# Optimization experiments

Hardware: AMD Instinct MI355X
Metric: run time of the kernel (lower is better)

Reference implementation:

```python
import jax, jax.numpy as jnp
import numpy as np

B, N, D, K = 16, 1024, 512, 8
NUM_ITERS = 3
EPS = 1e-08
LN_EPS = 1e-05


def layer_norm(x, g, b):
    m = jnp.mean(x, axis=-1, keepdims=True)
    v = jnp.var(x, axis=-1, keepdims=True)
    return (x - m) * jax.lax.rsqrt(v + LN_EPS) * g + b


def setup_inputs() -> dict:
    key = jax.random.key(0)
    ks = jax.random.split(key, 8)
    s = 1.0 / np.sqrt(D)
    return {
        "embeddings": jax.random.normal(ks[0], (B, N, D), jnp.float32),
        "noise_init": jax.random.normal(ks[1], (B, K, D), jnp.float32),
        "noise_final": jax.random.normal(ks[2], (B, K, D), jnp.float32),
        "slots_mu": jax.random.normal(ks[3], (1, K, D), jnp.float32) * s,
        "slots_logsigma": jax.random.normal(ks[4], (1, K, D), jnp.float32) * s,
        "mixing_coeffs": jnp.ones((1, K), jnp.float32) / K,
        "Wk": jax.random.normal(ks[5], (D, D), jnp.float32) * s,
        "bk": jnp.zeros((D,), jnp.float32),
        "Wq": jax.random.normal(ks[6], (D, D), jnp.float32) * s,
        "bq": jnp.zeros((D,), jnp.float32),
        "Wv": jax.random.normal(ks[7], (D, D), jnp.float32) * s,
        "bv": jnp.zeros((D,), jnp.float32),
        "ln_g": jnp.ones((D,), jnp.float32),
        "ln_b": jnp.zeros((D,), jnp.float32),
    }


def reference(embeddings, noise_init, noise_final, slots_mu, slots_logsigma,
              mixing_coeffs, Wk, bk, Wq, bq, Wv, bv, ln_g, ln_b):
    b, n, d = embeddings.shape
    mixing = jnp.broadcast_to(mixing_coeffs, (b, K))           # [B,K]
    mu = jnp.broadcast_to(slots_mu, (b, K, d))                 # [B,K,D]
    sigma = jnp.exp(jnp.broadcast_to(slots_logsigma, (b, K, d)))
    slots = mu + sigma * noise_init                            # sampled slots

    x = layer_norm(embeddings, ln_g, ln_b)
    keys = x @ Wk + bk                                         # [B,N,D]
    values = x @ Wv + bv                                       # [B,N,D]
    # slots are never updated inside the loop, so queries are loop-invariant
    queries = slots @ Wq + bq                                  # [B,K,D]

    log2pi = jnp.float32(np.log(2.0 * np.pi))
    attn = None
    for _ in range(NUM_ITERS):
        diff = keys[:, :, None, :] - queries[:, None, :, :]    # [B,N,K,D]
        gll = -0.5 * jnp.sum(diff * diff / (sigma[:, None] ** 2 + EPS), axis=-1)  # [B,N,K]
        gll = (-0.5 * d * log2pi
               - 0.5 * jnp.sum(jnp.log(jnp.abs(sigma) + EPS), axis=-1)[:, None, :]
               + gll)
        attn = mixing[:, None, :] * gll                        # [B,N,K]
        attn = attn / jnp.sum(attn, axis=-1, keepdims=True)
        attn = attn / (jnp.sum(attn, axis=1, keepdims=True) + EPS)
        mu = jnp.einsum('bnk,bnd->bkd', attn, values)          # [B,K,D]
        diff2 = values[:, :, None, :] - mu[:, None, :, :]      # [B,N,K,D]
        sigma = jnp.einsum('bnk,bnkd->bkd', attn, diff2 * diff2)
        mixing = jnp.sum(attn, axis=1) / n

    sigma = jnp.maximum(jnp.abs(sigma), EPS)
    slots = mu + sigma * noise_final
    return slots, jnp.transpose(attn, (0, 2, 1))
```

## Files before the change

kernel.cpp:

```cpp
#include <hip/hip_runtime.h>
#include <math.h>

#define BB 16
#define NN 1024
#define DD 512
#define KK 8
#define EPS_ 1e-8f
#define LN_EPS_ 1e-5f
#define GLL_C0 (-470.4965290007924f)

typedef __attribute__((ext_vector_type(8))) short short8;
typedef __attribute__((ext_vector_type(4))) short short4v;
typedef __attribute__((ext_vector_type(4))) float f32x4;

static __device__ inline short f2bf(float f) {
    unsigned u = __builtin_bit_cast(unsigned, f);
    u = (u + 0x7fff + ((u >> 16) & 1)) >> 16;
    return (short)u;
}
static __device__ inline float bf2f(short s) {
    unsigned u = ((unsigned)(unsigned short)s) << 16;
    return __builtin_bit_cast(float, u);
}

static __device__ inline void gload16(const void* g, void* l) {
    __builtin_amdgcn_global_load_lds(
        (const __attribute__((address_space(1))) void*)g,
        (__attribute__((address_space(3))) void*)l, 16, 0, 0);
}

__global__ __launch_bounds__(256) void pre_kernel(
    const float* __restrict__ emb, const float* __restrict__ lng,
    const float* __restrict__ lnb, short* __restrict__ Abf,
    const float* __restrict__ Wk, const float* __restrict__ Wv,
    const float* __restrict__ Wq, short* __restrict__ WtKV, short* __restrict__ WqT,
    const float* __restrict__ noise_init, const float* __restrict__ slots_mu,
    const float* __restrict__ slots_logsigma, short* __restrict__ slots_bf)
{
    int bid = blockIdx.x;
    int tid = threadIdx.x;
    if (bid < 4096) {
        int row  = bid * 4 + (tid >> 6);
        int lane = tid & 63;
        const float* e = emb + (size_t)row * DD + lane * 8;
        float4 v0 = *(const float4*)e;
        float4 v1 = *(const float4*)(e + 4);
        float v[8] = {v0.x, v0.y, v0.z, v0.w, v1.x, v1.y, v1.z, v1.w};
        float s = 0.0f;
#pragma unroll
        for (int j = 0; j < 8; j++) s += v[j];
#pragma unroll
        for (int off = 32; off; off >>= 1) s += __shfl_xor(s, off);
        float m = s * (1.0f / DD);
        float vs = 0.0f;
#pragma unroll
        for (int j = 0; j < 8; j++) { float d = v[j] - m; vs = fmaf(d, d, vs); }
#pragma unroll
        for (int off = 32; off; off >>= 1) vs += __shfl_xor(vs, off);
        float rstd = rsqrtf(vs * (1.0f / DD) + LN_EPS_);

        float4 g0 = *(const float4*)&lng[lane * 8];
        float4 g1 = *(const float4*)&lng[lane * 8 + 4];
        float4 b0 = *(const float4*)&lnb[lane * 8];
        float4 b1 = *(const float4*)&lnb[lane * 8 + 4];
        float g[8] = {g0.x, g0.y, g0.z, g0.w, g1.x, g1.y, g1.z, g1.w};
        float bb[8] = {b0.x, b0.y, b0.z, b0.w, b1.x, b1.y, b1.z, b1.w};
        short8 o;
#pragma unroll
        for (int j = 0; j < 8; j++) o[j] = f2bf(fmaf((v[j] - m) * rstd, g[j], bb[j]));
        *(short8*)&Abf[(size_t)row * DD + lane * 8] = o;
    } else if (bid < 4864) {
        int idx = bid - 4096;
        int z = idx >> 8, rem = idx & 255;
        const float* W = (z == 0) ? Wk : (z == 1) ? Wv : Wq;
        short* T; int nbase;
        if (z < 2) { T = WtKV; nbase = z * 512; } else { T = WqT; nbase = 0; }
        int k0 = (rem & 15) * 32, n0 = (rem >> 4) * 32;
        int tx = tid & 31, ty = tid >> 5;
        __shared__ float t[32][33];
#pragma unroll
        for (int p = 0; p < 4; p++)
            t[ty + p * 8][tx] = W[(size_t)(k0 + ty + p * 8) * DD + n0 + tx];
        __syncthreads();
#pragma unroll
        for (int p = 0; p < 4; p++)
            T[(size_t)(nbase + n0 + ty + p * 8) * DD + k0 + tx] = f2bf(t[tx][ty + p * 8]);
    } else {
        int idx = bid - 4864;
        int b = idx >> 3, k = idx & 7;
#pragma unroll
        for (int q = 0; q < 2; q++) {
            int d = tid + q * 256;
            float sg = expf(slots_logsigma[k * DD + d]);
            float sl = fmaf(sg, noise_init[((size_t)(b * KK + k)) * DD + d],
                            slots_mu[k * DD + d]);
            slots_bf[((size_t)(b * KK + k)) * DD + d] = f2bf(sl);
        }
    }
}

__global__ __launch_bounds__(256) void gemm_mfma_kernel(
    const short* __restrict__ Abf, const short* __restrict__ slotbf,
    const short* __restrict__ WtKV, const short* __restrict__ WqT,
    const float* __restrict__ bk, const float* __restrict__ bv,
    const float* __restrict__ bq,
    short* __restrict__ E, short* __restrict__ Vbf, float* __restrict__ Cq)
{
    int x = blockIdx.x, by = blockIdx.y;
    const short* A; const short* Bt;
    int qmode = 0, row0 = 0;
    if (by == 128) {
        if (x >= 4) return;
        A = slotbf; Bt = WqT; qmode = 1;
    } else {
        A = Abf + (size_t)by * 128 * DD;
        Bt = WtKV;
        row0 = by * 128;
    }

    __shared__ short As[128 * 64];
    __shared__ short Bs[128 * 64];

    int tid = threadIdx.x;
    int w = tid >> 6, l = tid & 63;
    int col0 = x * 128;

    int sr = l >> 3;
    int sg_off = ((l & 7) ^ sr) * 8;

    int mq = (w & 1) * 64, nq = (w >> 1) * 64;
    int fr = l & 15;

    f32x4 acc[4][4] = {};

    for (int k0 = 0; k0 < DD; k0 += 64) {
        __syncthreads();
#pragma unroll
        for (int j = 0; j < 4; j++) {
            int rb = w * 32 + j * 8;
            int r  = rb + sr;
            gload16(A  + (size_t)r * DD + k0 + sg_off, &As[rb * 64 + l * 8]);
            gload16(Bt + (size_t)(col0 + r) * DD + k0 + sg_off, &Bs[rb * 64 + l * 8]);
        }
        __syncthreads();

#pragma unroll
        for (int kk = 0; kk < 2; kk++) {
            int g = kk * 4 + (l >> 4);
            short8 af[4], bfv[4];
#pragma unroll
            for (int mi = 0; mi < 4; mi++) {
                int row = mq + mi * 16 + fr;
                af[mi] = *(const short8*)&As[row * 64 + (g ^ (fr & 7)) * 8];
            }
#pragma unroll
            for (int ni = 0; ni < 4; ni++) {
                int row = nq + ni * 16 + fr;
                bfv[ni] = *(const short8*)&Bs[row * 64 + (g ^ (fr & 7)) * 8];
            }
#pragma unroll
            for (int mi = 0; mi < 4; mi++)
#pragma unroll
                for (int ni = 0; ni < 4; ni++)
                    acc[mi][ni] = __builtin_amdgcn_mfma_f32_16x16x32_bf16(
                        af[mi], bfv[ni], acc[mi][ni], 0, 0, 0);
        }
    }

    int orow = (l >> 4) * 4, ocol = l & 15;
#pragma unroll
    for (int ni = 0; ni < 4; ni++) {
        int col = col0 + nq + ni * 16 + ocol;
        float bv_ = qmode ? bq[col] : (col < 512 ? bk[col] : bv[col - 512]);
#pragma unroll
        for (int mi = 0; mi < 4; mi++) {
#pragma unroll
            for (int r = 0; r < 4; r++) {
                int row = row0 + mq + mi * 16 + orow + r;
                float val = acc[mi][ni][r] + bv_;
                if (qmode) {
                    Cq[(size_t)row * DD + col] = val;
                } else if (col < 512) {
                    E[(size_t)row * 1024 + col]       = f2bf(val * val);
                    E[(size_t)row * 1024 + 512 + col] = f2bf(val);
                } else {
                    Vbf[(size_t)row * DD + (col - 512)] = f2bf(val);
                }
            }
        }
    }
}

__global__ __launch_bounds__(256) void fprep0_kernel(
    const float* __restrict__ slots_logsigma, const float* __restrict__ queries,
    const float* __restrict__ mixing_coeffs, short* __restrict__ F_bt,
    float* __restrict__ off, float* __restrict__ mix16, float* __restrict__ colsum)
{
    int b = blockIdx.x, k = blockIdx.y;
    int tid = threadIdx.x;
    short* Fr = F_bt + (size_t)(b * 16 + k) * 1024;
    if (k >= KK) {
        short4v zv = {0, 0, 0, 0};
        *(short4v*)&Fr[tid * 4] = zv;
        if (tid == 0) { off[b * 16 + k] = 0.0f; mix16[b * 16 + k] = 0.0f; }
        return;
    }
    float c = 0.0f, ld = 0.0f;
#pragma unroll
    for (int q = 0; q < 2; q++) {
        int d = tid * 2 + q;
        float sg = expf(slots_logsigma[k * DD + d]);
        float iv = 1.0f / (sg * sg + EPS_);
        float qv = queries[((size_t)(b * KK + k)) * DD + d];
        Fr[d]       = f2bf(-0.5f * iv);
        Fr[512 + d] = f2bf(qv * iv);
        c  = fmaf(qv * qv, iv, c);
        ld += logf(fabsf(sg) + EPS_);
    }
    __shared__ float rc[256], rl[256];
    rc[tid] = c; rl[tid] = ld;
    __syncthreads();
    for (int s = 128; s > 0; s >>= 1) {
        if (tid < s) { rc[tid] += rc[tid + s]; rl[tid] += rl[tid + s]; }
        __syncthreads();
    }
    if (tid == 0) {
        off[b * 16 + k]    = GLL_C0 - 0.5f * rl[0] - 0.5f * rc[0];
        mix16[b * 16 + k]  = mixing_coeffs[k];
        colsum[b * KK + k] = 0.0f;
    }
}

__global__ __launch_bounds__(256) void gll_mfma_kernel(
    const short* __restrict__ E, const short* __restrict__ F_bt,
    const float* __restrict__ off, const float* __restrict__ mix16,
    float* __restrict__ attn, float* __restrict__ colsum)
{
    int b = blockIdx.y;
    int tid = threadIdx.x;
    int w = tid >> 6, l = tid & 63;
    int m0 = blockIdx.x * 16;

    const short* Ea = E + ((size_t)(b * NN + m0 + (l & 15))) * 1024 + (l >> 4) * 8;
    const short* Fa = F_bt + (size_t)(b * 16 + (l & 15)) * 1024 + (l >> 4) * 8;

    f32x4 acc = {};
    int kbase = w * 256;
#pragma unroll
    for (int j = 0; j < 8; j++) {
        int k0 = kbase + j * 32;
        short8 af = *(const short8*)&Ea[k0];
        short8 bf = *(const short8*)&Fa[k0];
        acc = __builtin_amdgcn_mfma_f32_16x16x32_bf16(af, bf, acc, 0, 0, 0);
    }

    __shared__ f32x4 red[3][64];
    if (w) red[w - 1][l] = acc;
    __syncthreads();
    if (w) return;
#pragma unroll
    for (int i = 0; i < 3; i++) acc += red[i][l];

    int col = l & 15;
    int rbase = m0 + (l >> 4) * 4;
    float offv = off[b * 16 + col];
    float mixv = mix16[b * 16 + col];

    float a[4], den[4];
#pragma unroll
    for (int r = 0; r < 4; r++) {
        a[r] = mixv * (acc[r] + offv);
        den[r] = a[r];
    }
#pragma unroll
    for (int mask = 1; mask <= 8; mask <<= 1)
#pragma unroll
        for (int r = 0; r < 4; r++) den[r] += __shfl_xor(den[r], mask);

    float csl = 0.0f;
    if (col < KK) {
#pragma unroll
        for (int r = 0; r < 4; r++) {
            float v = a[r] / den[r];
            attn[((size_t)(b * NN + rbase + r)) * KK + col] = v;
            csl += v;
        }
    }
    csl += __shfl_xor(csl, 16);
    csl += __shfl_xor(csl, 32);
    if (l < KK) atomicAdd(&colsum[b * KK + l], csl);
}

__global__ __launch_bounds__(256) void musigma_kernel(
    const short* __restrict__ Vbf, const float* __restrict__ attn,
    float* __restrict__ s1p, float* __restrict__ s2p)
{
    int b = blockIdx.x, ns = blockIdx.y;
    int tid = threadIdx.x;
    int d0 = tid * 2;
    __shared__ float asml[64 * KK];
    const float* ab = attn + ((size_t)(b * NN + ns * 64)) * KK;
    if (tid < 128) ((float4*)asml)[tid] = ((const float4*)ab)[tid];
    __syncthreads();

    float s1[2][KK] = {}, s2[2][KK] = {};
    const short* vb = Vbf + ((size_t)(b * NN + ns * 64)) * DD + d0;
#pragma unroll 4
    for (int nn = 0; nn < 64; nn++) {
        short2 vs = *(const short2*)&vb[(size_t)nn * DD];
        float v0 = bf2f(vs.x), v1 = bf2f(vs.y);
        float v0q = v0 * v0, v1q = v1 * v1;
#pragma unroll
        for (int k = 0; k < KK; k++) {
            float a = asml[nn * KK + k];
            s1[0][k] = fmaf(a, v0, s1[0][k]);
            s2[0][k] = fmaf(a, v0q, s2[0][k]);
            s1[1][k] = fmaf(a, v1, s1[1][k]);
            s2[1][k] = fmaf(a, v1q, s2[1][k]);
        }
    }
    size_t base = ((size_t)(b * 16 + ns) * KK) * DD + d0;
#pragma unroll
    for (int k = 0; k < KK; k++) {
        *(float2*)&s1p[base + (size_t)k * DD] = make_float2(s1[0][k], s1[1][k]);
        *(float2*)&s2p[base + (size_t)k * DD] = make_float2(s2[0][k], s2[1][k]);
    }
}

__global__ __launch_bounds__(256) void fprep_fused_kernel(
    const float* __restrict__ s1p, const float* __restrict__ s2p,
    const float* __restrict__ queries, float* __restrict__ colsum,
    short* __restrict__ F_bt, float* __restrict__ off, float* __restrict__ mix16)
{
    int b = blockIdx.x, k = blockIdx.y;
    int tid = threadIdx.x;
    float cs   = colsum[b * KK + k];
    float inv  = 1.0f / (cs + EPS_);
    float ssum = cs * inv;
    short* Fr = F_bt + (size_t)(b * 16 + k) * 1024;

    float c = 0.0f, ld = 0.0f;
#pragma unroll
    for (int q = 0; q < 2; q++) {
        int d = tid * 2 + q;
        float s1 = 0.0f, s2 = 0.0f;
#pragma unroll
        for (int ns = 0; ns < 16; ns++) {
            size_t o = ((size_t)(b * 16 + ns) * KK + k) * DD + d;
            s1 += s1p[o];
            s2 += s2p[o];
        }
        float m  = s1 * inv;
        float sg = s2 * inv - m * m * (2.0f - ssum);
        float iv = 1.0f / (sg * sg + EPS_);
        float qv = queries[((size_t)(b * KK + k)) * DD + d];
        Fr[d]       = f2bf(-0.5f * iv);
        Fr[512 + d] = f2bf(qv * iv);
        c  = fmaf(qv * qv, iv, c);
        ld += logf(fabsf(sg) + EPS_);
    }
    __shared__ float rc[256], rl[256];
    rc[tid] = c; rl[tid] = ld;
    __syncthreads();
    for (int s = 128; s > 0; s >>= 1) {
        if (tid < s) { rc[tid] += rc[tid + s]; rl[tid] += rl[tid + s]; }
        __syncthreads();
    }
    if (tid == 0) {
        off[b * 16 + k]    = GLL_C0 - 0.5f * rl[0] - 0.5f * rc[0];
        mix16[b * 16 + k]  = ssum * (1.0f / NN);
        colsum[b * KK + k] = 0.0f;
    }
}

__global__ __launch_bounds__(256) void final_kernel(
    const float* __restrict__ s1p, const float* __restrict__ s2p,
    const float* __restrict__ colsum, const float* __restrict__ noise_final,
    const float* __restrict__ attn, float* __restrict__ out)
{
    int gid = blockIdx.x * 256 + threadIdx.x;
    if (gid < BB * KK * DD) {
        int d = gid & 511;
        int k = (gid >> 9) & 7;
        int b = gid >> 12;
        float s1 = 0.0f, s2 = 0.0f;
#pragma unroll
        for (int ns = 0; ns < 16; ns++) {
            size_t o = ((size_t)(b * 16 + ns) * KK + k) * DD + d;
            s1 += s1p[o];
            s2 += s2p[o];
        }
        float cs   = colsum[b * KK + k];
        float inv  = 1.0f / (cs + EPS_);
        float ssum = cs * inv;
        float m    = s1 * inv;
        float sg   = s2 * inv - m * m * (2.0f - ssum);
        out[gid] = fmaf(fmaxf(fabsf(sg), EPS_), noise_final[gid], m);
    }
    if (gid < BB * KK * NN) {
        int b = gid >> 13;
        int k = (gid >> 10) & 7;
        int n = gid & 1023;
        float cs = colsum[b * KK + k];
        out[BB * KK * DD + gid] = attn[((size_t)(b * NN + n)) * KK + k] / (cs + EPS_);
    }
}

extern "C" void kernel_launch(void* const* d_in, const int* in_sizes, int n_in,
                              void* d_out, int out_size, void* d_ws, size_t ws_size,
                              hipStream_t stream)
{
    const float* emb         = (const float*)d_in[0];
    const float* noise_init  = (const float*)d_in[1];
    const float* noise_final = (const float*)d_in[2];
    const float* slots_mu    = (const float*)d_in[3];
    const float* slots_logsg = (const float*)d_in[4];
    const float* mixing_co   = (const float*)d_in[5];
    const float* Wk          = (const float*)d_in[6];
    const float* bk          = (const float*)d_in[7];
    const float* Wq          = (const float*)d_in[8];
    const float* bq          = (const float*)d_in[9];
    const float* Wv          = (const float*)d_in[10];
    const float* bv          = (const float*)d_in[11];
    const float* ln_g        = (const float*)d_in[12];
    const float* ln_b        = (const float*)d_in[13];
    float* out = (float*)d_out;

    float* ws = (float*)d_ws;
    float* queries = ws;
    float* attn    = queries + BB * KK * DD;
    float* s1p     = attn + BB * NN * KK;
    float* s2p     = s1p + (size_t)BB * 16 * KK * DD;
    float* off     = s2p + (size_t)BB * 16 * KK * DD;
    float* mix16   = off + BB * 16;
    float* colsum  = mix16 + BB * 16;
    short* Abf     = (short*)(colsum + BB * KK);
    short* E       = Abf + (size_t)BB * NN * DD;
    short* Vbf     = E + (size_t)BB * NN * 1024;
    short* WtKV    = Vbf + (size_t)BB * NN * DD;
    short* WqT     = WtKV + (size_t)1024 * DD;
    short* slotbf  = WqT + (size_t)DD * DD;
    short* F_bt    = slotbf + (size_t)BB * KK * DD;

    pre_kernel<<<4992, 256, 0, stream>>>(
        emb, ln_g, ln_b, Abf, Wk, Wv, Wq, WtKV, WqT,
        noise_init, slots_mu, slots_logsg, slotbf);

    gemm_mfma_kernel<<<dim3(8, 129), 256, 0, stream>>>(
        Abf, slotbf, WtKV, WqT, bk, bv, bq, E, Vbf, queries);

    fprep0_kernel<<<dim3(BB, 16), 256, 0, stream>>>(
        slots_logsg, queries, mixing_co, F_bt, off, mix16, colsum);

    for (int it = 0; it < 3; it++) {
        gll_mfma_kernel<<<dim3(64, BB), 256, 0, stream>>>(
            E, F_bt, off, mix16, attn, colsum);
        musigma_kernel<<<dim3(BB, 16), 256, 0, stream>>>(Vbf, attn, s1p, s2p);
        if (it < 2)
            fprep_fused_kernel<<<dim3(BB, KK), 256, 0, stream>>>(
                s1p, s2p, queries, colsum, F_bt, off, mix16);
    }

    final_kernel<<<BB * KK * NN / 256, 256, 0, stream>>>(
        s1p, s2p, colsum, noise_final, attn, out);
}
```

Baseline: 243.8 us.

## Fuse all stages into one persistent cooperative kernel with grid syncs

Replaces the chain of about a dozen kernel launches with a single cooperative persistent kernel. It loops over work units per stage and separates stages with grid-wide barriers, and falls back to separate launches if the cooperative launch fails. The GEMM epilogue now stages bf16 outputs through swizzled shared memory so E and V are written with 16-byte coalesced stores instead of scattered 2-byte stores. The aim is to remove launch gaps and improve store efficiency. In exchange, each stage is limited to a fixed grid of 512 blocks, and grid syncs plus a large shared buffer may reduce occupancy.

```diff
diff --git a/kernel.cpp b/kernel.cpp
--- a/kernel.cpp
+++ b/kernel.cpp
@@ -1,5 +1,8 @@
 #include <hip/hip_runtime.h>
+#include <hip/hip_cooperative_groups.h>
 #include <math.h>
+
+namespace cg = cooperative_groups;
 
 #define BB 16
 #define NN 1024
@@ -22,27 +25,28 @@
     unsigned u = ((unsigned)(unsigned short)s) << 16;
     return __builtin_bit_cast(float, u);
 }
-
 static __device__ inline void gload16(const void* g, void* l) {
     __builtin_amdgcn_global_load_lds(
         (const __attribute__((address_space(1))) void*)g,
         (__attribute__((address_space(3))) void*)l, 16, 0, 0);
 }
 
-__global__ __launch_bounds__(256) void pre_kernel(
-    const float* __restrict__ emb, const float* __restrict__ lng,
-    const float* __restrict__ lnb, short* __restrict__ Abf,
-    const float* __restrict__ Wk, const float* __restrict__ Wv,
-    const float* __restrict__ Wq, short* __restrict__ WtKV, short* __restrict__ WqT,
-    const float* __restrict__ noise_init, const float* __restrict__ slots_mu,
-    const float* __restrict__ slots_logsigma, short* __restrict__ slots_bf)
-{
-    int bid = blockIdx.x;
-    int tid = threadIdx.x;
-    if (bid < 4096) {
-        int row  = bid * 4 + (tid >> 6);
+struct Params {
+    const float *emb, *noise_init, *noise_final, *slots_mu, *slots_logsg,
+                *mixing_co, *Wk, *bk, *Wq, *bq, *Wv, *bv, *ln_g, *ln_b;
+    float *out;
+    float *queries, *attn, *s1p, *s2p, *off, *mix16, *colsum;
+    short *Abf, *E, *Vbf, *WtKV, *WqT, *slotbf, *F_bt;
+};
+
+
+static __device__ __forceinline__ void do_pre(const Params& p, int u, int tid,
+                                              short* eb)
+{
+    if (u < 4096) {
+        int row  = u * 4 + (tid >> 6);
         int lane = tid & 63;
-        const float* e = emb + (size_t)row * DD + lane * 8;
+        const float* e = p.emb + (size_t)row * DD + lane * 8;
         float4 v0 = *(const float4*)e;
         float4 v1 = *(const float4*)(e + 4);
         float v[8] = {v0.x, v0.y, v0.z, v0.w, v1.x, v1.y, v1.z, v1.w};
@@ -59,80 +63,69 @@
         for (int off = 32; off; off >>= 1) vs += __shfl_xor(vs, off);
         float rstd = rsqrtf(vs * (1.0f / DD) + LN_EPS_);
 
-        float4 g0 = *(const float4*)&lng[lane * 8];
-        float4 g1 = *(const float4*)&lng[lane * 8 + 4];
-        float4 b0 = *(const float4*)&lnb[lane * 8];
-        float4 b1 = *(const float4*)&lnb[lane * 8 + 4];
+        float4 g0 = *(const float4*)&p.ln_g[lane * 8];
+        float4 g1 = *(const float4*)&p.ln_g[lane * 8 + 4];
+        float4 b0 = *(const float4*)&p.ln_b[lane * 8];
+        float4 b1 = *(const float4*)&p.ln_b[lane * 8 + 4];
         float g[8] = {g0.x, g0.y, g0.z, g0.w, g1.x, g1.y, g1.z, g1.w};
         float bb[8] = {b0.x, b0.y, b0.z, b0.w, b1.x, b1.y, b1.z, b1.w};
         short8 o;
 #pragma unroll
         for (int j = 0; j < 8; j++) o[j] = f2bf(fmaf((v[j] - m) * rstd, g[j], bb[j]));
-        *(short8*)&Abf[(size_t)row * DD + lane * 8] = o;
-    } else if (bid < 4864) {
-        int idx = bid - 4096;
+        *(short8*)&p.Abf[(size_t)row * DD + lane * 8] = o;
+    } else if (u < 4864) {
+        int idx = u - 4096;
         int z = idx >> 8, rem = idx & 255;
-        const float* W = (z == 0) ? Wk : (z == 1) ? Wv : Wq;
+        const float* W = (z == 0) ? p.Wk : (z == 1) ? p.Wv : p.Wq;
         short* T; int nbase;
-        if (z < 2) { T = WtKV; nbase = z * 512; } else { T = WqT; nbase = 0; }
+        if (z < 2) { T = p.WtKV; nbase = z * 512; } else { T = p.WqT; nbase = 0; }
         int k0 = (rem & 15) * 32, n0 = (rem >> 4) * 32;
         int tx = tid & 31, ty = tid >> 5;
-        __shared__ float t[32][33];
-#pragma unroll
-        for (int p = 0; p < 4; p++)
-            t[ty + p * 8][tx] = W[(size_t)(k0 + ty + p * 8) * DD + n0 + tx];
-        __syncthreads();
-#pragma unroll
-        for (int p = 0; p < 4; p++)
-            T[(size_t)(nbase + n0 + ty + p * 8) * DD + k0 + tx] = f2bf(t[tx][ty + p * 8]);
+        float (*t)[33] = (float (*)[33])eb;
+        __syncthreads();
+#pragma unroll
+        for (int q = 0; q < 4; q++)
+            t[ty + q * 8][tx] = W[(size_t)(k0 + ty + q * 8) * DD + n0 + tx];
+        __syncthreads();
+#pragma unroll
+        for (int q = 0; q < 4; q++)
+            T[(size_t)(nbase + n0 + ty + q * 8) * DD + k0 + tx] = f2bf(t[tx][ty + q * 8]);
+        __syncthreads();
     } else {
-        int idx = bid - 4864;
+        int idx = u - 4864;
         int b = idx >> 3, k = idx & 7;
 #pragma unroll
         for (int q = 0; q < 2; q++) {
             int d = tid + q * 256;
-            float sg = expf(slots_logsigma[k * DD + d]);
-            float sl = fmaf(sg, noise_init[((size_t)(b * KK + k)) * DD + d],
-                            slots_mu[k * DD + d]);
-            slots_bf[((size_t)(b * KK + k)) * DD + d] = f2bf(sl);
-        }
-    }
-}
-
-__global__ __launch_bounds__(256) void gemm_mfma_kernel(
-    const short* __restrict__ Abf, const short* __restrict__ slotbf,
-    const short* __restrict__ WtKV, const short* __restrict__ WqT,
-    const float* __restrict__ bk, const float* __restrict__ bv,
-    const float* __restrict__ bq,
-    short* __restrict__ E, short* __restrict__ Vbf, float* __restrict__ Cq)
-{
-    int x = blockIdx.x, by = blockIdx.y;
-    const short* A; const short* Bt;
-    int qmode = 0, row0 = 0;
-    if (by == 128) {
-        if (x >= 4) return;
-        A = slotbf; Bt = WqT; qmode = 1;
-    } else {
-        A = Abf + (size_t)by * 128 * DD;
-        Bt = WtKV;
-        row0 = by * 128;
-    }
-
-    __shared__ short As[128 * 64];
-    __shared__ short Bs[128 * 64];
-
-    int tid = threadIdx.x;
+            float sg = expf(p.slots_logsg[k * DD + d]);
+            float sl = fmaf(sg, p.noise_init[((size_t)(b * KK + k)) * DD + d],
+                            p.slots_mu[k * DD + d]);
+            p.slotbf[((size_t)(b * KK + k)) * DD + d] = f2bf(sl);
+        }
+    }
+}
+
+static __device__ __forceinline__ void do_gemm(const Params& p, int u, int tid,
+                                               short* eb)
+{
     int w = tid >> 6, l = tid & 63;
+    int x = u & 7, by = u >> 3;
+    int qmode = (by == 128);
+    if (qmode && x >= 4) return;
+    const short* A  = qmode ? p.slotbf : p.Abf + (size_t)by * 128 * DD;
+    const short* Bt = qmode ? p.WqT : p.WtKV;
+    int row0 = qmode ? 0 : by * 128;
     int col0 = x * 128;
 
+    short* As = eb;
+    short* Bs = eb + 8192;
     int sr = l >> 3;
     int sg_off = ((l & 7) ^ sr) * 8;
-
     int mq = (w & 1) * 64, nq = (w >> 1) * 64;
     int fr = l & 15;
+    int orow = (l >> 4) * 4, ocol = l & 15;
 
     f32x4 acc[4][4] = {};
-
     for (int k0 = 0; k0 < DD; k0 += 64) {
         __syncthreads();
 #pragma unroll
@@ -143,21 +136,16 @@
             gload16(Bt + (size_t)(col0 + r) * DD + k0 + sg_off, &Bs[rb * 64 + l * 8]);
         }
         __syncthreads();
-
 #pragma unroll
         for (int kk = 0; kk < 2; kk++) {
             int g = kk * 4 + (l >> 4);
             short8 af[4], bfv[4];
 #pragma unroll
-            for (int mi = 0; mi < 4; mi++) {
-                int row = mq + mi * 16 + fr;
-                af[mi] = *(const short8*)&As[row * 64 + (g ^ (fr & 7)) * 8];
-            }
-#pragma unroll
-            for (int ni = 0; ni < 4; ni++) {
-                int row = nq + ni * 16 + fr;
-                bfv[ni] = *(const short8*)&Bs[row * 64 + (g ^ (fr & 7)) * 8];
-            }
+            for (int mi = 0; mi < 4; mi++)
+                af[mi] = *(const short8*)&As[(mq + mi * 16 + fr) * 64 + (g ^ (fr & 7)) * 8];
+#pragma unroll
+            for (int ni = 0; ni < 4; ni++)
+                bfv[ni] = *(const short8*)&Bs[(nq + ni * 16 + fr) * 64 + (g ^ (fr & 7)) * 8];
 #pragma unroll
             for (int mi = 0; mi < 4; mi++)
 #pragma unroll
@@ -167,57 +155,89 @@
         }
     }
 
-    int orow = (l >> 4) * 4, ocol = l & 15;
+    float bvv[4];
 #pragma unroll
     for (int ni = 0; ni < 4; ni++) {
         int col = col0 + nq + ni * 16 + ocol;
-        float bv_ = qmode ? bq[col] : (col < 512 ? bk[col] : bv[col - 512]);
-#pragma unroll
-        for (int mi = 0; mi < 4; mi++) {
-#pragma unroll
-            for (int r = 0; r < 4; r++) {
-                int row = row0 + mq + mi * 16 + orow + r;
-                float val = acc[mi][ni][r] + bv_;
-                if (qmode) {
-                    Cq[(size_t)row * DD + col] = val;
-                } else if (col < 512) {
-                    E[(size_t)row * 1024 + col]       = f2bf(val * val);
-                    E[(size_t)row * 1024 + 512 + col] = f2bf(val);
+        bvv[ni] = qmode ? p.bq[col] : (x < 4 ? p.bk[col] : p.bv[col - 512]);
+    }
+
+    __syncthreads();
+    if (qmode) {
+#pragma unroll
+        for (int ni = 0; ni < 4; ni++) {
+            int col = col0 + nq + ni * 16 + ocol;
+#pragma unroll
+            for (int mi = 0; mi < 4; mi++)
+#pragma unroll
+                for (int r = 0; r < 4; r++)
+                    p.queries[(size_t)(mq + mi * 16 + orow + r) * DD + col] =
+                        acc[mi][ni][r] + bvv[ni];
+        }
+    } else {
+        int npass = (x < 4) ? 2 : 1;
+        for (int pass = 0; pass < npass; pass++) {
+#pragma unroll
+            for (int mi = 0; mi < 4; mi++)
+#pragma unroll
+                for (int r = 0; r < 4; r++) {
+                    int row = mq + mi * 16 + orow + r;
+                    int sw = ((row >> 2) & 3) << 1;
+#pragma unroll
+                    for (int ni = 0; ni < 4; ni++) {
+                        int colg = nq + ni * 16 + ocol;
+                        float val = acc[mi][ni][r] + bvv[ni];
+                        if (x < 4 && pass == 0) val = val * val;
+                        eb[row * 128 + (((colg >> 3) ^ sw) * 8) + (colg & 7)] = f2bf(val);
+                    }
+                }
+            __syncthreads();
+#pragma unroll
+            for (int i = 0; i < 8; i++) {
+                int row = i * 16 + w * 4 + (l >> 4);
+                int c = l & 15;
+                int cc = c ^ (((row >> 2) & 3) << 1);
+                short8 vv = *(const short8*)&eb[row * 128 + cc * 8];
+                if (x < 4) {
+                    size_t a = (size_t)(row0 + row) * 1024 +
+                               (pass ? 512 + col0 : col0) + c * 8;
+                    *(short8*)&p.E[a] = vv;
                 } else {
-                    Vbf[(size_t)row * DD + (col - 512)] = f2bf(val);
+                    *(short8*)&p.Vbf[(size_t)(row0 + row) * 512 +
+                                     (col0 - 512) + c * 8] = vv;
                 }
             }
-        }
-    }
-}
-
-__global__ __launch_bounds__(256) void fprep0_kernel(
-    const float* __restrict__ slots_logsigma, const float* __restrict__ queries,
-    const float* __restrict__ mixing_coeffs, short* __restrict__ F_bt,
-    float* __restrict__ off, float* __restrict__ mix16, float* __restrict__ colsum)
-{
-    int b = blockIdx.x, k = blockIdx.y;
-    int tid = threadIdx.x;
-    short* Fr = F_bt + (size_t)(b * 16 + k) * 1024;
+            __syncthreads();
+        }
+    }
+}
+
+static __device__ __forceinline__ void do_fprep0(const Params& p, int u, int tid,
+                                                 float* red)
+{
+    int b = u >> 4, k = u & 15;
+    short* Fr = p.F_bt + (size_t)(b * 16 + k) * 1024;
     if (k >= KK) {
         short4v zv = {0, 0, 0, 0};
         *(short4v*)&Fr[tid * 4] = zv;
-        if (tid == 0) { off[b * 16 + k] = 0.0f; mix16[b * 16 + k] = 0.0f; }
+        if (tid == 0) { p.off[b * 16 + k] = 0.0f; p.mix16[b * 16 + k] = 0.0f; }
         return;
     }
+    float* rc = red;
+    float* rl = red + 256;
     float c = 0.0f, ld = 0.0f;
 #pragma unroll
     for (int q = 0; q < 2; q++) {
         int d = tid * 2 + q;
-        float sg = expf(slots_logsigma[k * DD + d]);
+        float sg = expf(p.slots_logsg[k * DD + d]);
         float iv = 1.0f / (sg * sg + EPS_);
-        float qv = queries[((size_t)(b * KK + k)) * DD + d];
+        float qv = p.queries[((size_t)(b * KK + k)) * DD + d];
         Fr[d]       = f2bf(-0.5f * iv);
         Fr[512 + d] = f2bf(qv * iv);
         c  = fmaf(qv * qv, iv, c);
         ld += logf(fabsf(sg) + EPS_);
     }
-    __shared__ float rc[256], rl[256];
+    __syncthreads();
     rc[tid] = c; rl[tid] = ld;
     __syncthreads();
     for (int s = 128; s > 0; s >>= 1) {
@@ -225,25 +245,20 @@
         __syncthreads();
     }
     if (tid == 0) {
-        off[b * 16 + k]    = GLL_C0 - 0.5f * rl[0] - 0.5f * rc[0];
-        mix16[b * 16 + k]  = mixing_coeffs[k];
-        colsum[b * KK + k] = 0.0f;
-    }
-}
-
-__global__ __launch_bounds__(256) void gll_mfma_kernel(
-    const short* __restrict__ E, const short* __restrict__ F_bt,
-    const float* __restrict__ off, const float* __restrict__ mix16,
-    float* __restrict__ attn, float* __restrict__ colsum)
-{
-    int b = blockIdx.y;
-    int tid = threadIdx.x;
+        p.off[b * 16 + k]    = GLL_C0 - 0.5f * rl[0] - 0.5f * rc[0];
+        p.mix16[b * 16 + k]  = p.mixing_co[k];
+        p.colsum[b * KK + k] = 0.0f;
+    }
+}
+
+static __device__ __forceinline__ void do_gll(const Params& p, int u, int tid,
+                                              short* eb)
+{
     int w = tid >> 6, l = tid & 63;
-    int m0 = blockIdx.x * 16;
-
-    const short* Ea = E + ((size_t)(b * NN + m0 + (l & 15))) * 1024 + (l >> 4) * 8;
-    const short* Fa = F_bt + (size_t)(b * 16 + (l & 15)) * 1024 + (l >> 4) * 8;
-
+    int b = u >> 6;
+    int m0 = (u & 63) * 16;
+    const short* Ea = p.E + ((size_t)(b * NN + m0 + (l & 15))) * 1024 + (l >> 4) * 8;
+    const short* Fa = p.F_bt + (size_t)(b * 16 + (l & 15)) * 1024 + (l >> 4) * 8;
     f32x4 acc = {};
     int kbase = w * 256;
 #pragma unroll
@@ -253,58 +268,53 @@
         short8 bf = *(const short8*)&Fa[k0];
         acc = __builtin_amdgcn_mfma_f32_16x16x32_bf16(af, bf, acc, 0, 0, 0);
     }
-
-    __shared__ f32x4 red[3][64];
-    if (w) red[w - 1][l] = acc;
-    __syncthreads();
-    if (w) return;
-#pragma unroll
-    for (int i = 0; i < 3; i++) acc += red[i][l];
-
-    int col = l & 15;
-    int rbase = m0 + (l >> 4) * 4;
-    float offv = off[b * 16 + col];
-    float mixv = mix16[b * 16 + col];
-
-    float a[4], den[4];
-#pragma unroll
-    for (int r = 0; r < 4; r++) {
-        a[r] = mixv * (acc[r] + offv);
-        den[r] = a[r];
-    }
-#pragma unroll
-    for (int mask = 1; mask <= 8; mask <<= 1)
-#pragma unroll
-        for (int r = 0; r < 4; r++) den[r] += __shfl_xor(den[r], mask);
-
-    float csl = 0.0f;
-    if (col < KK) {
+    f32x4* red = (f32x4*)eb;
+    __syncthreads();
+    if (w) red[(w - 1) * 64 + l] = acc;
+    __syncthreads();
+    if (w == 0) {
+#pragma unroll
+        for (int i = 0; i < 3; i++) acc += red[i * 64 + l];
+        int col = l & 15;
+        int rbase = m0 + (l >> 4) * 4;
+        float offv = p.off[b * 16 + col];
+        float mixv = p.mix16[b * 16 + col];
+        float a[4], den[4];
 #pragma unroll
         for (int r = 0; r < 4; r++) {
-            float v = a[r] / den[r];
-            attn[((size_t)(b * NN + rbase + r)) * KK + col] = v;
-            csl += v;
-        }
-    }
-    csl += __shfl_xor(csl, 16);
-    csl += __shfl_xor(csl, 32);
-    if (l < KK) atomicAdd(&colsum[b * KK + l], csl);
-}
-
-__global__ __launch_bounds__(256) void musigma_kernel(
-    const short* __restrict__ Vbf, const float* __restrict__ attn,
-    float* __restrict__ s1p, float* __restrict__ s2p)
-{
-    int b = blockIdx.x, ns = blockIdx.y;
-    int tid = threadIdx.x;
+            a[r] = mixv * (acc[r] + offv);
+            den[r] = a[r];
+        }
+#pragma unroll
+        for (int mask = 1; mask <= 8; mask <<= 1)
+#pragma unroll
+            for (int r = 0; r < 4; r++) den[r] += __shfl_xor(den[r], mask);
+        float csl = 0.0f;
+        if (col < KK) {
+#pragma unroll
+            for (int r = 0; r < 4; r++) {
+                float vv = a[r] / den[r];
+                p.attn[((size_t)(b * NN + rbase + r)) * KK + col] = vv;
+                csl += vv;
+            }
+        }
+        csl += __shfl_xor(csl, 16);
+        csl += __shfl_xor(csl, 32);
+        if (l < KK) atomicAdd(&p.colsum[b * KK + l], csl);
+    }
+}
+
+static __device__ __forceinline__ void do_musigma(const Params& p, int u, int tid,
+                                                  float* asml)
+{
+    int b = u >> 4, ns = u & 15;
     int d0 = tid * 2;
-    __shared__ float asml[64 * KK];
-    const float* ab = attn + ((size_t)(b * NN + ns * 64)) * KK;
+    const float* ab = p.attn + ((size_t)(b * NN + ns * 64)) * KK;
+    __syncthreads();
     if (tid < 128) ((float4*)asml)[tid] = ((const float4*)ab)[tid];
     __syncthreads();
-
     float s1[2][KK] = {}, s2[2][KK] = {};
-    const short* vb = Vbf + ((size_t)(b * NN + ns * 64)) * DD + d0;
+    const short* vb = p.Vbf + ((size_t)(b * NN + ns * 64)) * DD + d0;
 #pragma unroll 4
     for (int nn = 0; nn < 64; nn++) {
         short2 vs = *(const short2*)&vb[(size_t)nn * DD];
@@ -322,23 +332,21 @@
     size_t base = ((size_t)(b * 16 + ns) * KK) * DD + d0;
 #pragma unroll
     for (int k = 0; k < KK; k++) {
-        *(float2*)&s1p[base + (size_t)k * DD] = make_float2(s1[0][k], s1[1][k]);
-        *(float2*)&s2p[base + (size_t)k * DD] = make_float2(s2[0][k], s2[1][k]);
-    }
-}
-
-__global__ __launch_bounds__(256) void fprep_fused_kernel(
-    const float* __restrict__ s1p, const float* __restrict__ s2p,
-    const float* __restrict__ queries, float* __restrict__ colsum,
-    short* __restrict__ F_bt, float* __restrict__ off, float* __restrict__ mix16)
-{
-    int b = blockIdx.x, k = blockIdx.y;
-    int tid = threadIdx.x;
-    float cs   = colsum[b * KK + k];
+        *(float2*)&p.s1p[base + (size_t)k * DD] = make_float2(s1[0][k], s1[1][k]);
+        *(float2*)&p.s2p[base + (size_t)k * DD] = make_float2(s2[0][k], s2[1][k]);
+    }
+}
+
+static __device__ __forceinline__ void do_fprep(const Params& p, int u, int tid,
+                                                float* red)
+{
+    int b = u >> 3, k = u & 7;
+    float cs   = p.colsum[b * KK + k];
     float inv  = 1.0f / (cs + EPS_);
     float ssum = cs * inv;
-    short* Fr = F_bt + (size_t)(b * 16 + k) * 1024;
-
+    short* Fr = p.F_bt + (size_t)(b * 16 + k) * 1024;
+    float* rc = red;
+    float* rl = red + 256;
     float c = 0.0f, ld = 0.0f;
 #pragma unroll
     for (int q = 0; q < 2; q++) {
@@ -347,19 +355,19 @@
 #pragma unroll
         for (int ns = 0; ns < 16; ns++) {
             size_t o = ((size_t)(b * 16 + ns) * KK + k) * DD + d;
-            s1 += s1p[o];
-            s2 += s2p[o];
+            s1 += p.s1p[o];
+            s2 += p.s2p[o];
         }
         float m  = s1 * inv;
         float sg = s2 * inv - m * m * (2.0f - ssum);
         float iv = 1.0f / (sg * sg + EPS_);
-        float qv = queries[((size_t)(b * KK + k)) * DD + d];
+        float qv = p.queries[((size_t)(b * KK + k)) * DD + d];
         Fr[d]       = f2bf(-0.5f * iv);
         Fr[512 + d] = f2bf(qv * iv);
         c  = fmaf(qv * qv, iv, c);
         ld += logf(fabsf(sg) + EPS_);
     }
-    __shared__ float rc[256], rl[256];
+    __syncthreads();
     rc[tid] = c; rl[tid] = ld;
     __syncthreads();
     for (int s = 128; s > 0; s >>= 1) {
@@ -367,19 +375,16 @@
         __syncthreads();
     }
     if (tid == 0) {
-        off[b * 16 + k]    = GLL_C0 - 0.5f * rl[0] - 0.5f * rc[0];
-        mix16[b * 16 + k]  = ssum * (1.0f / NN);
-        colsum[b * KK + k] = 0.0f;
-    }
-}
-
-__global__ __launch_bounds__(256) void final_kernel(
-    const float* __restrict__ s1p, const float* __restrict__ s2p,
-    const float* __restrict__ colsum, const float* __restrict__ noise_final,
-    const float* __restrict__ attn, float* __restrict__ out)
-{
-    int gid = blockIdx.x * 256 + threadIdx.x;
-    if (gid < BB * KK * DD) {
+        p.off[b * 16 + k]    = GLL_C0 - 0.5f * rl[0] - 0.5f * rc[0];
+        p.mix16[b * 16 + k]  = ssum * (1.0f / NN);
+        p.colsum[b * KK + k] = 0.0f;
+    }
+}
+
+static __device__ __forceinline__ void do_final(const Params& p, int u, int tid)
+{
+    if (u < 256) {
+        int gid = u * 256 + tid;
         int d = gid & 511;
         int k = (gid >> 9) & 7;
         int b = gid >> 12;
@@ -387,80 +392,132 @@
 #pragma unroll
         for (int ns = 0; ns < 16; ns++) {
             size_t o = ((size_t)(b * 16 + ns) * KK + k) * DD + d;
-            s1 += s1p[o];
-            s2 += s2p[o];
-        }
-        float cs   = colsum[b * KK + k];
+            s1 += p.s1p[o];
+            s2 += p.s2p[o];
+        }
+        float cs   = p.colsum[b * KK + k];
         float inv  = 1.0f / (cs + EPS_);
         float ssum = cs * inv;
         float m    = s1 * inv;
         float sg   = s2 * inv - m * m * (2.0f - ssum);
-        out[gid] = fmaf(fmaxf(fabsf(sg), EPS_), noise_final[gid], m);
-    }
-    if (gid < BB * KK * NN) {
+        p.out[gid] = fmaf(fmaxf(fabsf(sg), EPS_), p.noise_final[gid], m);
+    } else {
+        int gid = (u - 256) * 256 + tid;
         int b = gid >> 13;
         int k = (gid >> 10) & 7;
         int n = gid & 1023;
-        float cs = colsum[b * KK + k];
-        out[BB * KK * DD + gid] = attn[((size_t)(b * NN + n)) * KK + k] / (cs + EPS_);
-    }
+        float cs = p.colsum[b * KK + k];
+        p.out[BB * KK * DD + gid] =
+            p.attn[((size_t)(b * NN + n)) * KK + k] / (cs + EPS_);
+    }
+}
+
+__global__ __launch_bounds__(256, 2) void fused_kernel(Params p)
+{
+    cg::grid_group gg = cg::this_grid();
+    __shared__ __align__(16) short eb[128 * 128];
+    int bid = blockIdx.x, tid = threadIdx.x;
+    int G = gridDim.x;
+
+    for (int u = bid; u < 4992; u += G) do_pre(p, u, tid, eb);
+    gg.sync();
+    for (int u = bid; u < 1032; u += G) do_gemm(p, u, tid, eb);
+    gg.sync();
+    for (int u = bid; u < 256; u += G) do_fprep0(p, u, tid, (float*)eb);
+    gg.sync();
+    for (int it = 0; it < 3; it++) {
+        for (int u = bid; u < 1024; u += G) do_gll(p, u, tid, eb);
+        gg.sync();
+        for (int u = bid; u < 256; u += G) do_musigma(p, u, tid, (float*)eb);
+        gg.sync();
+        if (it < 2) {
+            for (int u = bid; u < 128; u += G) do_fprep(p, u, tid, (float*)eb);
+            gg.sync();
+        }
+    }
+    for (int u = bid; u < 768; u += G) do_final(p, u, tid);
+}
+
+__global__ __launch_bounds__(256) void k_pre(Params p) {
+    __shared__ __align__(16) short eb[4352];
+    do_pre(p, blockIdx.x, threadIdx.x, eb);
+}
+__global__ __launch_bounds__(256) void k_gemm(Params p) {
+    __shared__ __align__(16) short eb[128 * 128];
+    do_gemm(p, blockIdx.x, threadIdx.x, eb);
+}
+__global__ __launch_bounds__(256) void k_fprep0(Params p) {
+    __shared__ float red[512];
+    do_fprep0(p, blockIdx.x, threadIdx.x, red);
+}
+__global__ __launch_bounds__(256) void k_gll(Params p) {
+    __shared__ __align__(16) short eb[192 * 16];
+    do_gll(p, blockIdx.x, threadIdx.x, eb);
+}
+__global__ __launch_bounds__(256) void k_musigma(Params p) {
+    __shared__ float asml[512];
+    do_musigma(p, blockIdx.x, threadIdx.x, asml);
+}
+__global__ __launch_bounds__(256) void k_fprep(Params p) {
+    __shared__ float red[512];
+    do_fprep(p, blockIdx.x, threadIdx.x, red);
+}
+__global__ __launch_bounds__(256) void k_final(Params p) {
+    do_final(p, blockIdx.x, threadIdx.x);
 }
 
 extern "C" void kernel_launch(void* const* d_in, const int* in_sizes, int n_in,
                               void* d_out, int out_size, void* d_ws, size_t ws_size,
                               hipStream_t stream)
 {
-    const float* emb         = (const float*)d_in[0];
-    const float* noise_init  = (const float*)d_in[1];
-    const float* noise_final = (const float*)d_in[2];
-    const float* slots_mu    = (const float*)d_in[3];
-    const float* slots_logsg = (const float*)d_in[4];
-    const float* mixing_co   = (const float*)d_in[5];
-    const float* Wk          = (const float*)d_in[6];
-    const float* bk          = (const float*)d_in[7];
-    const float* Wq          = (const float*)d_in[8];
-    const float* bq          = (const float*)d_in[9];
-    const float* Wv          = (const float*)d_in[10];
-    const float* bv          = (const float*)d_in[11];
-    const float* ln_g        = (const float*)d_in[12];
-    const float* ln_b        = (const float*)d_in[13];
-    float* out = (float*)d_out;
+    Params pp;
+    pp.emb         = (const float*)d_in[0];
+    pp.noise_init  = (const float*)d_in[1];
+    pp.noise_final = (const float*)d_in[2];
+    pp.slots_mu    = (const float*)d_in[3];
+    pp.slots_logsg = (const float*)d_in[4];
+    pp.mixing_co   = (const float*)d_in[5];
+    pp.Wk          = (const float*)d_in[6];
+    pp.bk          = (const float*)d_in[7];
+    pp.Wq          = (const float*)d_in[8];
+    pp.bq          = (const float*)d_in[9];
+    pp.Wv          = (const float*)d_in[10];
+    pp.bv          = (const float*)d_in[11];
+    pp.ln_g        = (const float*)d_in[12];
+    pp.ln_b        = (const float*)d_in[13];
+    pp.out         = (float*)d_out;
 
     float* ws = (float*)d_ws;
-    float* queries = ws;
-    float* attn    = queries + BB * KK * DD;
-    float* s1p     = attn + BB * NN * KK;
-    float* s2p     = s1p + (size_t)BB * 16 * KK * DD;
-    float* off     = s2p + (size_t)BB * 16 * KK * DD;
-    float* mix16   = off + BB * 16;
-    float* colsum  = mix16 + BB * 16;
-    short* Abf     = (short*)(colsum + BB * KK);
-    short* E       = Abf + (size_t)BB * NN * DD;
-    short* Vbf     = E + (size_t)BB * NN * 1024;
-    short* WtKV    = Vbf + (size_t)BB * NN * DD;
-    short* WqT     = WtKV + (size_t)1024 * DD;
-    short* slotbf  = WqT + (size_t)DD * DD;
-    short* F_bt    = slotbf + (size_t)BB * KK * DD;
-
-    pre_kernel<<<4992, 256, 0, stream>>>(
-        emb, ln_g, ln_b, Abf, Wk, Wv, Wq, WtKV, WqT,
-        noise_init, slots_mu, slots_logsg, slotbf);
-
-    gemm_mfma_kernel<<<dim3(8, 129), 256, 0, stream>>>(
-        Abf, slotbf, WtKV, WqT, bk, bv, bq, E, Vbf, queries);
-
-    fprep0_kernel<<<dim3(BB, 16), 256, 0, stream>>>(
-        slots_logsg, queries, mixing_co, F_bt, off, mix16, colsum);
-
-    for (int it = 0; it < 3; it++) {
-        gll_mfma_kernel<<<dim3(64, BB), 256, 0, stream>>>(
-            E, F_bt, off, mix16, attn, colsum);
-        musigma_kernel<<<dim3(BB, 16), 256, 0, stream>>>(Vbf, attn, s1p, s2p);
-        if (it < 2)
-            fprep_fused_kernel<<<dim3(BB, KK), 256, 0, stream>>>(
-                s1p, s2p, queries, colsum, F_bt, off, mix16);
-    }
-
-    final_kernel<<<BB * KK * NN / 256, 256, 0, stream>>>(
-        s1p, s2p, colsum, noise_final, attn, out);
-}
+    pp.queries = ws;
+    pp.attn    = pp.queries + BB * KK * DD;
+    pp.s1p     = pp.attn + BB * NN * KK;
+    pp.s2p     = pp.s1p + (size_t)BB * 16 * KK * DD;
+    pp.off     = pp.s2p + (size_t)BB * 16 * KK * DD;
+    pp.mix16   = pp.off + BB * 16;
+    pp.colsum  = pp.mix16 + BB * 16;
+    pp.Abf     = (short*)(pp.colsum + BB * KK);
+    pp.E       = pp.Abf + (size_t)BB * NN * DD;
+    pp.Vbf     = pp.E + (size_t)BB * NN * 1024;
+    pp.WtKV    = pp.Vbf + (size_t)BB * NN * DD;
+    pp.WqT     = pp.WtKV + (size_t)1024 * DD;
+    pp.slotbf  = pp.WqT + (size_t)DD * DD;
+    pp.F_bt    = pp.slotbf + (size_t)BB * KK * DD;
+
+    void* args[] = { (void*)&pp };
+    hipError_t e = hipLaunchCooperativeKernel((const void*)fused_kernel,
+                                              dim3(512), dim3(256), args, 0, stream);
+    if (e != hipSuccess)
+        e = hipLaunchCooperativeKernel((const void*)fused_kernel,
+                                       dim3(256), dim3(256), args, 0, stream);
+    if (e != hipSuccess) {
+        k_pre<<<4992, 256, 0, stream>>>(pp);
+        k_gemm<<<1032, 256, 0, stream>>>(pp);
+        k_fprep0<<<256, 256, 0, stream>>>(pp);
+        for (int it = 0; it < 3; it++) {
+            k_gll<<<1024, 256, 0, stream>>>(pp);
+            k_musigma<<<256, 256, 0, stream>>>(pp);
+            if (it < 2) k_fprep<<<128, 256, 0, stream>>>(pp);
+        }
+        k_final<<<768, 256, 0, stream>>>(pp);
+    }
+}
```

New measurement: 867.0 us. +255.6%, slower.
